# Kernel tuning notes

Hardware: AMD Instinct MI355X
Metric: run time of the kernel (lower is better)

## Reference

```python
import jax, jax.numpy as jnp
import numpy as np

L, N, E, D, H, B = 4, 50000, 800000, 128, 64, 16384
ED = 2 * D  # edge_dim
K = 7      # conv1d kernel size


def setup_inputs() -> dict:
    key = jax.random.key(0)
    ks = jax.random.split(key, 12)
    return {
        "x_nodes": jax.random.normal(ks[0], (L, N, 1), jnp.float32),
        "edge_index": jax.random.randint(ks[1], (L, 2, E), 0, N),
        "W1": jax.random.normal(ks[2], (L, 1, H), jnp.float32) * 0.1,
        "b1": jnp.zeros((L, H), jnp.float32),
        "gamma": jnp.ones((L, H), jnp.float32),
        "beta": jnp.zeros((L, H), jnp.float32),
        "W2": jax.random.normal(ks[3], (L, H, D), jnp.float32) * 0.05,
        "b2": jnp.zeros((L, D), jnp.float32),
        "conv_w": jax.random.normal(ks[4], (ED, ED, K), jnp.float32) * 0.02,
        "conv_b": jnp.zeros((ED,), jnp.float32),
        "lc_w": jax.random.normal(ks[5], (ED, L), jnp.float32) * 0.05,
        "lc_b": jnp.zeros((L,), jnp.float32),
        "link_w": jax.random.normal(ks[6], (ED, 2), jnp.float32) * 0.05,
        "link_b": jnp.zeros((2,), jnp.float32),
        "now_layer": jax.random.randint(ks[7], (B,), 0, L),
        "leftnode": jax.random.randint(ks[8], (B,), 0, N),
        "rightnode": jax.random.randint(ks[9], (B,), 0, N),
    }


def gcn_conv(x, src, dst, norm, W, b):
    # x: [N, Fin] -> [N, Fout]; symmetric-normalized message passing (GCNConv)
    xw = x @ W
    out = jax.ops.segment_sum(norm[:, None] * xw[src], dst, num_segments=N)
    return out + b


def gcn_layer(x, ei, W1, b1, g, bt, W2, b2):
    loops = jnp.arange(N, dtype=ei.dtype)
    src = jnp.concatenate([ei[0], loops])
    dst = jnp.concatenate([ei[1], loops])
    deg = jax.ops.segment_sum(jnp.ones_like(src, jnp.float32), dst, num_segments=N)
    dis = jax.lax.rsqrt(jnp.maximum(deg, 1e-12))
    norm = dis[src] * dis[dst]
    h = gcn_conv(x, src, dst, norm, W1, b1)
    # BatchNorm1d (training mode: batch stats over nodes)
    mu = h.mean(axis=0)
    var = h.var(axis=0)
    h = g * (h - mu) * jax.lax.rsqrt(var + 1e-5) + bt
    h = jax.nn.relu(h)
    return gcn_conv(h, src, dst, norm, W2, b2)


def reference(x_nodes, edge_index, W1, b1, gamma, beta, W2, b2,
              conv_w, conv_b, lc_w, lc_b, link_w, link_b,
              now_layer, leftnode, rightnode):
    # Per-layer GCN embeddings (fixed small L -> Python loop is fine, keeps peak memory low)
    embeds = jnp.stack([
        gcn_layer(x_nodes[i], edge_index[i], W1[i], b1[i], gamma[i], beta[i], W2[i], b2[i])
        for i in range(L)
    ])  # [L, N, D]

    # Edge features: gather per-sample layer-specific node embeddings and concat
    left = embeds[now_layer, leftnode]    # [B, D]
    right = embeds[now_layer, rightnode]  # [B, D]
    layer_specific = jnp.concatenate([left, right], axis=-1)  # [B, ED]

    # Conv1d applied unbatched on [ED, B] (convolves across batch dim, as in original)
    dn = jax.lax.conv_dimension_numbers((1, ED, B), (ED, ED, K), ('NCH', 'OIH', 'NCH'))
    y = jax.lax.conv_general_dilated(layer_specific.T[None], conv_w, (1,), [(3, 3)],
                                     dimension_numbers=dn)[0]  # [ED, B]
    shared = jax.nn.relu(y + conv_b[:, None]).T  # [B, ED]

    discriminant_outs = shared @ lc_w + lc_b  # [B, L]

    # Ortho_algorithm: remove shared component from specific, combine with shared
    dot = jnp.sum(layer_specific * shared, axis=-1, keepdims=True)
    nrm = jnp.sum(shared * shared, axis=-1, keepdims=True)
    enhanced = layer_specific - (dot / (nrm + 1e-12)) * shared + shared  # [B, ED]

    prediction_outs = enhanced @ link_w + link_b  # [B, 2]
    return prediction_outs, discriminant_outs
```

## Files before the change

kernel.cpp:

```cpp
#include <hip/hip_runtime.h>
#include <hip/hip_bf16.h>

#define Lc 4
#define Nc 50000
#define Ec 800000
#define Bc 16384
#define EDc 256
#define Kc 7
#define Mtot (Lc * Nc)
#define KDIM (EDc * Kc)

#define BINW 512
#define BSH 9
#define FB 98
#define NBINS (FB * Lc)
#define CAPc 12288
#define CHUNK 8192
#define FBLK ((Ec + CHUNK - 1) / CHUNK)

#define PADTOT 33024
#define PADBIT (1 << 24)

typedef __attribute__((ext_vector_type(8))) short bf16x8;
typedef __attribute__((ext_vector_type(4))) float f32x4;

static __device__ __forceinline__ unsigned short f2bf(float f) {
    unsigned u = __float_as_uint(f);
    unsigned r = (u + 0x7fffu + ((u >> 16) & 1u)) >> 16;
    return (unsigned short)r;
}
static __device__ __forceinline__ float bf2f(unsigned short u) {
    return __uint_as_float(((unsigned)u) << 16);
}


__global__ __launch_bounds__(1024) void k_binfill(const int* __restrict__ ei,
                                                  int* __restrict__ binCursor,
                                                  int* __restrict__ binned) {
    int l = blockIdx.y;
    int e0 = blockIdx.x * CHUNK;
    __shared__ int lh[FB], lcur[FB];
    if (threadIdx.x < FB) lh[threadIdx.x] = 0;
    __syncthreads();
    const int* srcp = ei + (size_t)l * 2 * Ec;
    const int* dstp = srcp + Ec;
#pragma unroll
    for (int it = 0; it < CHUNK / 1024; it++) {
        int idx = e0 + it * 1024 + threadIdx.x;
        if (idx < Ec) atomicAdd(&lh[dstp[idx] >> BSH], 1);
    }
    __syncthreads();
    if (threadIdx.x < FB) {
        int c = lh[threadIdx.x];
        int bin = l * FB + threadIdx.x;
        int st = c ? atomicAdd(&binCursor[bin], c) : 0;
        lcur[threadIdx.x] = bin * CAPc + min(st, CAPc);
        lh[threadIdx.x] = bin * CAPc + CAPc;
    }
    __syncthreads();
#pragma unroll
    for (int it = 0; it < CHUNK / 1024; it++) {
        int idx = e0 + it * 1024 + threadIdx.x;
        if (idx < Ec) {
            int d = dstp[idx], sv = srcp[idx];
            int t = d >> BSH;
            int pos = atomicAdd(&lcur[t], 1);
            if (pos < lh[t]) binned[pos] = (sv << BSH) | (d & (BINW - 1));
        }
    }
}

__global__ void k_mark(const int* __restrict__ now, const int* __restrict__ lnn,
                       const int* __restrict__ rnn, int* __restrict__ ord,
                       unsigned* __restrict__ bitmap, int* __restrict__ gcnt) {
    int b = blockIdx.x * 256 + threadIdx.x;
    for (int p = b; p < PADTOT; p += 16384) ord[p] = PADBIT;
    int l = now[b];
    int a1 = l * Nc + lnn[b];
    atomicOr(&bitmap[a1 >> 5], 1u << (a1 & 31));
    int a2 = l * Nc + rnn[b];
    atomicOr(&bitmap[a2 >> 5], 1u << (a2 & 31));
    int lane = threadIdx.x & 63;
#pragma unroll
    for (int ll = 0; ll < 4; ll++) {
        unsigned long long m = __ballot(l == ll);
        if (m && lane == __builtin_ctzll(m)) atomicAdd(&gcnt[ll], __popcll(m));
    }
}

__global__ void k_order2(const int* __restrict__ now, const int* __restrict__ gcnt,
                         int* __restrict__ gcur, int* __restrict__ ord) {
    int b = blockIdx.x * 256 + threadIdx.x;
    int l = now[b];
    int segBase = 0;
    for (int ll = 0; ll < l; ll++) segBase += (2 * gcnt[ll] + 63) & ~63;
    int lane = threadIdx.x & 63;
#pragma unroll
    for (int ll = 0; ll < 4; ll++) {
        unsigned long long m = __ballot(l == ll);
        if (!m) continue;
        int ldr = __builtin_ctzll(m);
        int bs = 0;
        if (lane == ldr) bs = atomicAdd(&gcur[ll], __popcll(m));
        bs = __shfl(bs, ldr);
        if (l == ll) {
            int rk = __popcll(m & (lane ? ((1ull << lane) - 1) : 0ull));
            int sp = segBase + 2 * (bs + rk);
            ord[sp] = (2 * b) | (ll << 20);
            ord[sp + 1] = (2 * b + 1) | (ll << 20);
        }
    }
}

__global__ __launch_bounds__(512) void k_csr(const int* __restrict__ binCnt,
                                             const int* __restrict__ binned,
                                             const float* __restrict__ x_nodes,
                                             const unsigned* __restrict__ bitmap,
                                             int* __restrict__ csr,
                                             int* __restrict__ rstart,
                                             int* __restrict__ cnt,
                                             float* __restrict__ dis,
                                             float* __restrict__ g) {
    int b = blockIdx.x;
    int l = b / FB, gg = b % FB;
    int rs = b * CAPc;
    int cntb = binCnt[b];
    if (cntb > CAPc) cntb = CAPc;
    int re = rs + cntb;
    __shared__ int hist[BINW];
    hist[threadIdx.x] = 0;
    __syncthreads();
    for (int i = rs + threadIdx.x; i < re; i += 512)
        atomicAdd(&hist[binned[i] & (BINW - 1)], 1);
    __syncthreads();
    int lane = threadIdx.x & 63, wid = threadIdx.x >> 6;
    int v = hist[threadIdx.x];
    int x = v;
#pragma unroll
    for (int off = 1; off < 64; off <<= 1) {
        int y = __shfl_up(x, off);
        if (lane >= off) x += y;
    }
    __shared__ int ws[8];
    if (lane == 63) ws[wid] = x;
    __syncthreads();
    int carry = 0;
    for (int w = 0; w < wid; w++) carry += ws[w];
    int exc = x - v + carry;
    int n = gg * BINW + threadIdx.x;
    int n4 = l * Nc + n;
    if (n < Nc) {
        rstart[n4] = rs + exc;
        cnt[n4] = v;
        float dn = rsqrtf((float)v + 1.0f);
        dis[n4] = dn;
        g[n4] = dn * x_nodes[(size_t)l * Nc + n];
    }
    __syncthreads();
    hist[threadIdx.x] = rs + exc;
    __syncthreads();
    int lbase = l * Nc + gg * BINW;
    for (int i = rs + threadIdx.x; i < re; i += 512) {
        unsigned p = (unsigned)binned[i];
        int d = p & (BINW - 1);
        int nn4 = lbase + d;
        if ((bitmap[nn4 >> 5] >> (nn4 & 31)) & 1u) {
            int pos = atomicAdd(&hist[d], 1);
            csr[pos] = (int)(p >> BSH);
        }
    }
}

__global__ __launch_bounds__(512) void k_s_bin(const int* __restrict__ binCnt,
                                               const int* __restrict__ binned,
                                               const float* __restrict__ g,
                                               const float* __restrict__ dis,
                                               float2* __restrict__ ns,
                                               double* __restrict__ stats) {
    int b = blockIdx.x;
    int l = b / FB, gg = b % FB;
    int rs = b * CAPc;
    int cntb = binCnt[b];
    if (cntb > CAPc) cntb = CAPc;
    int re = rs + cntb;
    const float* gl = g + (size_t)l * Nc;
    __shared__ float acc[BINW];
    acc[threadIdx.x] = 0.f;
    __syncthreads();
    for (int i = rs + threadIdx.x; i < re; i += 512) {
        unsigned p = (unsigned)binned[i];
        atomicAdd(&acc[p & (BINW - 1)], gl[p >> BSH]);
    }
    __syncthreads();
    int n = gg * BINW + threadIdx.x;
    int n4 = l * Nc + n;
    double v = 0.0, v2 = 0.0;
    if (n < Nc) {
        float dn = dis[n4];
        float sf = dn * (acc[threadIdx.x] + g[n4]);
        ns[n4] = make_float2(dn, sf);
        v = (double)sf;
        v2 = (double)sf * (double)sf;
    }
    for (int m = 32; m; m >>= 1) { v += __shfl_xor(v, m); v2 += __shfl_xor(v2, m); }
    __shared__ double r0[8], r1[8];
    int wid = threadIdx.x >> 6, lane = threadIdx.x & 63;
    if (lane == 0) { r0[wid] = v; r1[wid] = v2; }
    __syncthreads();
    if (threadIdx.x == 0) {
        double a = 0, bb = 0;
        for (int w = 0; w < 8; w++) { a += r0[w]; bb += r1[w]; }
        atomicAdd(&stats[l * 2 + 0], a);
        atomicAdd(&stats[l * 2 + 1], bb);
    }
}

__global__ void k_cvec4(const double* __restrict__ stats, const float* __restrict__ W1,
                        const float* __restrict__ gamma, float* __restrict__ cbuf) {
    int l = threadIdx.x >> 6, h = threadIdx.x & 63;
    double mean = stats[l * 2] / (double)Nc;
    double var = stats[l * 2 + 1] / (double)Nc - mean * mean;
    float w = W1[l * 64 + h];
    cbuf[l * 72 + h] = gamma[l * 64 + h] * w * rsqrtf((float)var * w * w + 1e-5f);
    if (h == 0) cbuf[l * 72 + 64] = (float)mean;
}


__global__ __launch_bounds__(256) void k_agg(const int* __restrict__ ord,
        const int* __restrict__ lnn, const int* __restrict__ rnn,
        const int* __restrict__ rstart, const int* __restrict__ cnt,
        const int* __restrict__ csr, const float2* __restrict__ ns,
        const float* __restrict__ cbuf, const float* __restrict__ beta,
        unsigned short* __restrict__ acch) {
    int pos = blockIdx.x * 4 + (threadIdx.x >> 6);
    int lane = threadIdx.x & 63;
    int ordv = ord[pos];
    if (ordv & PADBIT) { acch[(size_t)pos * 64 + lane] = 0; return; }
    int side = ordv & 0xFFFFF;
    int l = (ordv >> 20) & 3;
    int b = side >> 1;
    int n = (side & 1) ? rnn[b] : lnn[b];
    int n4 = l * Nc + n;
    float c = cbuf[l * 72 + lane], mu = cbuf[l * 72 + 64], bt = beta[l * 64 + lane];
    const float2* nsl = ns + (size_t)l * Nc;
    int st = rstart[n4], deg = cnt[n4];
    float a = 0.f;
    for (int base = 0; base < deg; base += 64) {
        int e = base + lane;
        int sv = (e < deg) ? csr[st + e] : 0;
        float nv = 0.f, fv = 0.f;
        if (e < deg) {
            float2 nf = nsl[sv];
            nv = nf.x; fv = nf.y;
        }
        int m = min(64, deg - base);
        for (int j = 0; j < m; j++) {
            float nj = __shfl(nv, j);
            float fj = __shfl(fv, j);
            a += nj * fmaxf(c * (fj - mu) + bt, 0.f);
        }
    }
    float2 nself = ns[n4];
    float hs = fmaxf(c * (nself.y - mu) + bt, 0.f);
    a = nself.x * a + nself.x * nself.x * hs;
    acch[(size_t)pos * 64 + lane] = f2bf(a);
}

__global__ __launch_bounds__(256) void k_embgemm(const unsigned short* __restrict__ acch,
        const int* __restrict__ ord, const unsigned short* __restrict__ w2t,
        const float* __restrict__ b2, unsigned short* __restrict__ lsh) {
    int t0 = blockIdx.x * 16;
    int wn = threadIdx.x >> 6, lane = threadIdx.x & 63;
    int lrow = lane & 15, lg = lane >> 4;
    int l = (ord[t0] >> 20) & 3;
    const unsigned short* ap = acch + (size_t)(t0 + lrow) * 64 + lg * 8;
    const unsigned short* bp = w2t + (size_t)(l * 128 + wn * 32 + lrow) * 64 + lg * 8;
    f32x4 acc[2] = {};
#pragma unroll
    for (int kt = 0; kt < 2; kt++) {
        bf16x8 a = *(const bf16x8*)(ap + kt * 32);
        bf16x8 b0 = *(const bf16x8*)(bp + kt * 32);
        bf16x8 b1 = *(const bf16x8*)(bp + 16 * 64 + kt * 32);
        acc[0] = __builtin_amdgcn_mfma_f32_16x16x32_bf16(a, b0, acc[0], 0, 0, 0);
        acc[1] = __builtin_amdgcn_mfma_f32_16x16x32_bf16(a, b1, acc[1], 0, 0, 0);
    }
#pragma unroll
    for (int r = 0; r < 4; r++) {
        int pos = t0 + lg * 4 + r;
        int ordv = ord[pos];
        if (ordv & PADBIT) continue;
        int side = ordv & 0xFFFFF;
        size_t base = (size_t)(side >> 1) * 256 + (side & 1) * 128;
#pragma unroll
        for (int ni = 0; ni < 2; ni++) {
            int n = wn * 32 + ni * 16 + lrow;
            lsh[base + n] = f2bf(acc[ni][r] + b2[l * 128 + n]);
        }
    }
}


__global__ void k_wbf(const float* __restrict__ w, unsigned short* __restrict__ wbt) {
    int i = blockIdx.x * 256 + threadIdx.x;
    int co = i / KDIM;
    int r = i % KDIM;
    int ci = r / Kc, k = r % Kc;
    wbt[(size_t)co * KDIM + k * EDc + ci] = f2bf(w[i]);
}

__global__ void k_w2t(const float* __restrict__ W2, unsigned short* __restrict__ w2t,
                      int* __restrict__ zeroRegion, int zn) {
    int i = blockIdx.x * 256 + threadIdx.x;
    if (i < zn) zeroRegion[i] = 0;
    int l = i >> 13, r = i & 8191;
    int d = r >> 6, h = r & 63;
    w2t[i] = f2bf(W2[(size_t)(l * 64 + h) * 128 + d]);
}

__global__ __launch_bounds__(512, 1) void k_convmma(const unsigned short* __restrict__ lsh,
                                                    const unsigned short* __restrict__ wbt,
                                                    const float* __restrict__ cb,
                                                    float* __restrict__ sh) {
    __shared__ unsigned short lsa[70 * EDc];
    int b0 = blockIdx.x * 64;
    int wid = threadIdx.x >> 6, lane = threadIdx.x & 63;
    int lrow = lane & 15, lg = lane >> 4;

    for (int idx = threadIdx.x; idx < 70 * 32; idx += 512) {
        int r = idx >> 5, c = idx & 31;
        int grow = b0 - 3 + r;
        uint4 v = make_uint4(0u, 0u, 0u, 0u);
        if ((unsigned)grow < (unsigned)Bc)
            v = *(const uint4*)(lsh + (size_t)grow * EDc + c * 8);
        int byte = (r * 512 + c * 16) ^ ((r & 7) << 4);
        *(uint4*)((char*)lsa + byte) = v;
    }
    __syncthreads();

    const unsigned short* w0 = wbt + (size_t)(wid * 32 + lrow) * KDIM + lg * 8;

    f32x4 acc[4][2] = {};
    bf16x8 br0[8][2], br1[8][2];

#pragma unroll
    for (int tt = 0; tt < 8; tt++)
#pragma unroll
        for (int ni = 0; ni < 2; ni++)
            br0[tt][ni] = *(const bf16x8*)(w0 + ni * 16 * KDIM + tt * 32);

#pragma unroll
    for (int k = 0; k < Kc; k++) {
        if (k < Kc - 1) {
#pragma unroll
            for (int tt = 0; tt < 8; tt++)
#pragma unroll
                for (int ni = 0; ni < 2; ni++) {
                    bf16x8 v = *(const bf16x8*)(w0 + ni * 16 * KDIM + (k + 1) * 256 + tt * 32);
                    if (k & 1) br0[tt][ni] = v; else br1[tt][ni] = v;
                }
        }
#pragma unroll
        for (int tt = 0; tt < 8; tt++) {
            bf16x8 a[4];
#pragma unroll
            for (int mi = 0; mi < 4; mi++) {
                int l = mi * 16 + lrow + k;
                a[mi] = *(const bf16x8*)((const char*)lsa + l * 512
                        + ((lg * 16 + tt * 64) ^ ((l & 7) << 4)));
            }
#pragma unroll
            for (int mi = 0; mi < 4; mi++)
#pragma unroll
                for (int ni = 0; ni < 2; ni++) {
                    bf16x8 bv = (k & 1) ? br1[tt][ni] : br0[tt][ni];
                    acc[mi][ni] = __builtin_amdgcn_mfma_f32_16x16x32_bf16(
                        a[mi], bv, acc[mi][ni], 0, 0, 0);
                }
        }
    }

#pragma unroll
    for (int mi = 0; mi < 4; mi++) {
        int rbase = b0 + mi * 16 + lg * 4;
#pragma unroll
        for (int ni = 0; ni < 2; ni++) {
            int co = wid * 32 + ni * 16 + lrow;
            float bias = cb[co];
#pragma unroll
            for (int r = 0; r < 4; r++)
                sh[(size_t)(rbase + r) * EDc + co] = fmaxf(acc[mi][ni][r] + bias, 0.0f);
        }
    }
}

__global__ __launch_bounds__(256) void k_final(const unsigned short* __restrict__ lsh,
                        const float* __restrict__ sh,
                        const float* __restrict__ lc_w, const float* __restrict__ lc_b,
                        const float* __restrict__ link_w, const float* __restrict__ link_b,
                        float* __restrict__ out) {
    int b = blockIdx.x * 4 + (threadIdx.x >> 6);
    int lane = threadIdx.x & 63;
    float lsv[4], shv[4];
    float dot = 0.f, nrm = 0.f;
#pragma unroll
    for (int i = 0; i < 4; i++) {
        int ci = lane + i * 64;
        lsv[i] = bf2f(lsh[(size_t)b * 256 + ci]);
        shv[i] = sh[(size_t)b * 256 + ci];
        dot += lsv[i] * shv[i];
        nrm += shv[i] * shv[i];
    }
    for (int m = 32; m; m >>= 1) { dot += __shfl_xor(dot, m); nrm += __shfl_xor(nrm, m); }
    float coef = dot / (nrm + 1e-12f);
    float p0 = 0.f, p1 = 0.f, d0 = 0.f, d1 = 0.f, d2 = 0.f, d3 = 0.f;
#pragma unroll
    for (int i = 0; i < 4; i++) {
        int ci = lane + i * 64;
        float e = lsv[i] - coef * shv[i] + shv[i];
        p0 += e * link_w[ci * 2];
        p1 += e * link_w[ci * 2 + 1];
        d0 += shv[i] * lc_w[ci * 4];
        d1 += shv[i] * lc_w[ci * 4 + 1];
        d2 += shv[i] * lc_w[ci * 4 + 2];
        d3 += shv[i] * lc_w[ci * 4 + 3];
    }
    for (int m = 32; m; m >>= 1) {
        p0 += __shfl_xor(p0, m); p1 += __shfl_xor(p1, m);
        d0 += __shfl_xor(d0, m); d1 += __shfl_xor(d1, m);
        d2 += __shfl_xor(d2, m); d3 += __shfl_xor(d3, m);
    }
    if (lane == 0) {
        out[b * 2]     = p0 + link_b[0];
        out[b * 2 + 1] = p1 + link_b[1];
        float* dd = out + 2 * Bc;
        dd[b * 4]     = d0 + lc_b[0];
        dd[b * 4 + 1] = d1 + lc_b[1];
        dd[b * 4 + 2] = d2 + lc_b[2];
        dd[b * 4 + 3] = d3 + lc_b[3];
    }
}


extern "C" void kernel_launch(void* const* d_in, const int* in_sizes, int n_in,
                              void* d_out, int out_size, void* d_ws, size_t ws_size,
                              hipStream_t stream) {
    const float* x_nodes    = (const float*)d_in[0];
    const int*   edge_index = (const int*)d_in[1];
    const float* W1   = (const float*)d_in[2];
    const float* gamma = (const float*)d_in[4];
    const float* beta  = (const float*)d_in[5];
    const float* W2   = (const float*)d_in[6];
    const float* b2   = (const float*)d_in[7];
    const float* conv_w = (const float*)d_in[8];
    const float* conv_b = (const float*)d_in[9];
    const float* lc_w   = (const float*)d_in[10];
    const float* lc_b   = (const float*)d_in[11];
    const float* link_w = (const float*)d_in[12];
    const float* link_b = (const float*)d_in[13];
    const int* now = (const int*)d_in[14];
    const int* ln  = (const int*)d_in[15];
    const int* rn  = (const int*)d_in[16];
    float* out = (float*)d_out;

    char* base = (char*)d_ws;
    size_t off = 0;
    auto carve = [&](size_t bytes) {
        void* p = base + off;
        off = (off + bytes + 255) & ~(size_t)255;
        return p;
    };
    int*      binCursor = (int*)carve(NBINS * 4);
    int*      gcnt      = (int*)carve(4 * 4);
    int*      gcur      = (int*)carve(4 * 4);
    unsigned* bitmap    = (unsigned*)carve(6272 * 4);
    double*   stats     = (double*)carve(8 * 8);
    int*    binned    = (int*)carve((size_t)NBINS * CAPc * 4);
    int*    rstart    = (int*)carve((size_t)Mtot * 4);
    int*    cnt       = (int*)carve((size_t)Mtot * 4);
    int*    csr       = (int*)carve((size_t)NBINS * CAPc * 4);
    float*  dis       = (float*)carve((size_t)Mtot * 4);
    float*  g         = (float*)carve((size_t)Mtot * 4);
    float2* ns        = (float2*)carve((size_t)Mtot * 8);
    float*  cbuf      = (float*)carve(Lc * 72 * 4);
    int*    ord       = (int*)carve((size_t)PADTOT * 4);
    unsigned short* acch = (unsigned short*)carve((size_t)PADTOT * 64 * 2);
    float*  shb       = (float*)carve((size_t)Bc * 256 * 4);
    unsigned short* lsh = (unsigned short*)carve((size_t)Bc * 256 * 2);
    unsigned short* wbt = (unsigned short*)carve((size_t)EDc * KDIM * 2);
    unsigned short* w2t = (unsigned short*)carve((size_t)Lc * 128 * 64 * 2);
    (void)ws_size;

    int zn = (int)(((char*)(stats + 8) - (char*)binCursor) / 4);

    k_w2t<<<128, 256, 0, stream>>>(W2, w2t, binCursor, zn);
    k_wbf<<<1792, 256, 0, stream>>>(conv_w, wbt);
    k_mark<<<64, 256, 0, stream>>>(now, ln, rn, ord, bitmap, gcnt);

    k_binfill<<<dim3(FBLK, Lc), 1024, 0, stream>>>(edge_index, binCursor, binned);
    k_csr<<<NBINS, 512, 0, stream>>>(binCursor, binned, x_nodes, bitmap,
                                     csr, rstart, cnt, dis, g);
    k_s_bin<<<NBINS, 512, 0, stream>>>(binCursor, binned, g, dis, ns, stats);
    k_cvec4<<<1, 256, 0, stream>>>(stats, W1, gamma, cbuf);
    k_order2<<<64, 256, 0, stream>>>(now, gcnt, gcur, ord);
    k_agg<<<PADTOT / 4, 256, 0, stream>>>(ord, ln, rn, rstart, cnt, csr, ns,
                                          cbuf, beta, acch);
    k_embgemm<<<PADTOT / 16, 256, 0, stream>>>(acch, ord, w2t, b2, lsh);

    k_convmma<<<Bc / 64, 512, 0, stream>>>(lsh, wbt, conv_b, shb);
    k_final<<<Bc / 4, 256, 0, stream>>>(lsh, shb, lc_w, lc_b, link_w, link_b, out);
}
```

Measured before the change: 179.0 us.

## Fuse pipeline kernels to cut launches and intermediate global buffers

Merges the weight-prep kernels into one launch and folds the sample-marking pass into an extra block of the edge-binning kernel. The layer-order and BN-coefficient kernels become one launch. Aggregation and the W2 MFMA GEMM are fused so the aggregated rows stay in shared memory instead of a global bf16 buffer. The conv MFMA kernel now also runs the orthogonal-projection/linear heads from shared memory, removing the shared-feature global round trip. The costs are a single serial block doing the sample marking, larger 1024-thread blocks for aggregation, and extra LDS for the conv block (64x256 floats).

After: 202.0 us. 12.8% more time.

```diff
diff --git a/kernel.cpp b/kernel.cpp
--- a/kernel.cpp
+++ b/kernel.cpp
@@ -34,9 +34,53 @@
 }
 
 
+__global__ void k_prep(const float* __restrict__ conv_w, unsigned short* __restrict__ wbt,
+                       const float* __restrict__ W2, unsigned short* __restrict__ w2t,
+                       int* __restrict__ zeroRegion, int zn) {
+    int bb = blockIdx.x;
+    if (bb < 1792) {
+        int i = bb * 256 + threadIdx.x;
+        int co = i / KDIM;
+        int r = i % KDIM;
+        int ci = r / Kc, k = r % Kc;
+        wbt[(size_t)co * KDIM + k * EDc + ci] = f2bf(conv_w[i]);
+    } else {
+        int i = (bb - 1792) * 256 + threadIdx.x;
+        if (i < zn) zeroRegion[i] = 0;
+        int l = i >> 13, r = i & 8191;
+        int d = r >> 6, h = r & 63;
+        w2t[i] = f2bf(W2[(size_t)(l * 64 + h) * 128 + d]);
+    }
+}
+
+
 __global__ __launch_bounds__(1024) void k_binfill(const int* __restrict__ ei,
                                                   int* __restrict__ binCursor,
-                                                  int* __restrict__ binned) {
+                                                  int* __restrict__ binned,
+                                                  const int* __restrict__ now,
+                                                  const int* __restrict__ lnn,
+                                                  const int* __restrict__ rnn,
+                                                  int* __restrict__ ord,
+                                                  unsigned* __restrict__ bitmap,
+                                                  int* __restrict__ gcnt) {
+    if (blockIdx.x == FBLK) {
+        if (blockIdx.y != 0) return;
+        int lane = threadIdx.x & 63;
+        for (int p = threadIdx.x; p < PADTOT; p += 1024) ord[p] = PADBIT;
+        for (int b = threadIdx.x; b < Bc; b += 1024) {
+            int l = now[b];
+            int a1 = l * Nc + lnn[b];
+            atomicOr(&bitmap[a1 >> 5], 1u << (a1 & 31));
+            int a2 = l * Nc + rnn[b];
+            atomicOr(&bitmap[a2 >> 5], 1u << (a2 & 31));
+#pragma unroll
+            for (int ll = 0; ll < 4; ll++) {
+                unsigned long long m = __ballot(l == ll);
+                if (m && lane == __builtin_ctzll(m)) atomicAdd(&gcnt[ll], __popcll(m));
+            }
+        }
+        return;
+    }
     int l = blockIdx.y;
     int e0 = blockIdx.x * CHUNK;
     __shared__ int lh[FB], lcur[FB];
@@ -66,48 +110,6 @@
             int t = d >> BSH;
             int pos = atomicAdd(&lcur[t], 1);
             if (pos < lh[t]) binned[pos] = (sv << BSH) | (d & (BINW - 1));
-        }
-    }
-}
-
-__global__ void k_mark(const int* __restrict__ now, const int* __restrict__ lnn,
-                       const int* __restrict__ rnn, int* __restrict__ ord,
-                       unsigned* __restrict__ bitmap, int* __restrict__ gcnt) {
-    int b = blockIdx.x * 256 + threadIdx.x;
-    for (int p = b; p < PADTOT; p += 16384) ord[p] = PADBIT;
-    int l = now[b];
-    int a1 = l * Nc + lnn[b];
-    atomicOr(&bitmap[a1 >> 5], 1u << (a1 & 31));
-    int a2 = l * Nc + rnn[b];
-    atomicOr(&bitmap[a2 >> 5], 1u << (a2 & 31));
-    int lane = threadIdx.x & 63;
-#pragma unroll
-    for (int ll = 0; ll < 4; ll++) {
-        unsigned long long m = __ballot(l == ll);
-        if (m && lane == __builtin_ctzll(m)) atomicAdd(&gcnt[ll], __popcll(m));
-    }
-}
-
-__global__ void k_order2(const int* __restrict__ now, const int* __restrict__ gcnt,
-                         int* __restrict__ gcur, int* __restrict__ ord) {
-    int b = blockIdx.x * 256 + threadIdx.x;
-    int l = now[b];
-    int segBase = 0;
-    for (int ll = 0; ll < l; ll++) segBase += (2 * gcnt[ll] + 63) & ~63;
-    int lane = threadIdx.x & 63;
-#pragma unroll
-    for (int ll = 0; ll < 4; ll++) {
-        unsigned long long m = __ballot(l == ll);
-        if (!m) continue;
-        int ldr = __builtin_ctzll(m);
-        int bs = 0;
-        if (lane == ldr) bs = atomicAdd(&gcur[ll], __popcll(m));
-        bs = __shfl(bs, ldr);
-        if (l == ll) {
-            int rk = __popcll(m & (lane ? ((1ull << lane) - 1) : 0ull));
-            int sp = segBase + 2 * (bs + rk);
-            ord[sp] = (2 * b) | (ll << 20);
-            ord[sp + 1] = (2 * b + 1) | (ll << 20);
         }
     }
 }
@@ -215,113 +217,123 @@
     }
 }
 
-__global__ void k_cvec4(const double* __restrict__ stats, const float* __restrict__ W1,
-                        const float* __restrict__ gamma, float* __restrict__ cbuf) {
-    int l = threadIdx.x >> 6, h = threadIdx.x & 63;
-    double mean = stats[l * 2] / (double)Nc;
-    double var = stats[l * 2 + 1] / (double)Nc - mean * mean;
-    float w = W1[l * 64 + h];
-    cbuf[l * 72 + h] = gamma[l * 64 + h] * w * rsqrtf((float)var * w * w + 1e-5f);
-    if (h == 0) cbuf[l * 72 + 64] = (float)mean;
-}
-
-
-__global__ __launch_bounds__(256) void k_agg(const int* __restrict__ ord,
+
+__global__ __launch_bounds__(256) void k_ordcvec(const int* __restrict__ now,
+        const int* __restrict__ gcnt, int* __restrict__ gcur, int* __restrict__ ord,
+        const double* __restrict__ stats, const float* __restrict__ W1,
+        const float* __restrict__ gamma, float* __restrict__ cbuf) {
+    if (blockIdx.x == 64) {
+        int l = threadIdx.x >> 6, h = threadIdx.x & 63;
+        double mean = stats[l * 2] / (double)Nc;
+        double var = stats[l * 2 + 1] / (double)Nc - mean * mean;
+        float w = W1[l * 64 + h];
+        cbuf[l * 72 + h] = gamma[l * 64 + h] * w * rsqrtf((float)var * w * w + 1e-5f);
+        if (h == 0) cbuf[l * 72 + 64] = (float)mean;
+        return;
+    }
+    int b = blockIdx.x * 256 + threadIdx.x;
+    int l = now[b];
+    int segBase = 0;
+    for (int ll = 0; ll < l; ll++) segBase += (2 * gcnt[ll] + 63) & ~63;
+    int lane = threadIdx.x & 63;
+#pragma unroll
+    for (int ll = 0; ll < 4; ll++) {
+        unsigned long long m = __ballot(l == ll);
+        if (!m) continue;
+        int ldr = __builtin_ctzll(m);
+        int bs = 0;
+        if (lane == ldr) bs = atomicAdd(&gcur[ll], __popcll(m));
+        bs = __shfl(bs, ldr);
+        if (l == ll) {
+            int rk = __popcll(m & (lane ? ((1ull << lane) - 1) : 0ull));
+            int sp = segBase + 2 * (bs + rk);
+            ord[sp] = (2 * b) | (ll << 20);
+            ord[sp + 1] = (2 * b + 1) | (ll << 20);
+        }
+    }
+}
+
+
+__global__ __launch_bounds__(1024) void k_aggemm(const int* __restrict__ ord,
         const int* __restrict__ lnn, const int* __restrict__ rnn,
         const int* __restrict__ rstart, const int* __restrict__ cnt,
         const int* __restrict__ csr, const float2* __restrict__ ns,
         const float* __restrict__ cbuf, const float* __restrict__ beta,
-        unsigned short* __restrict__ acch) {
-    int pos = blockIdx.x * 4 + (threadIdx.x >> 6);
-    int lane = threadIdx.x & 63;
-    int ordv = ord[pos];
-    if (ordv & PADBIT) { acch[(size_t)pos * 64 + lane] = 0; return; }
-    int side = ordv & 0xFFFFF;
-    int l = (ordv >> 20) & 3;
-    int b = side >> 1;
-    int n = (side & 1) ? rnn[b] : lnn[b];
-    int n4 = l * Nc + n;
-    float c = cbuf[l * 72 + lane], mu = cbuf[l * 72 + 64], bt = beta[l * 64 + lane];
-    const float2* nsl = ns + (size_t)l * Nc;
-    int st = rstart[n4], deg = cnt[n4];
+        const unsigned short* __restrict__ w2t, const float* __restrict__ b2,
+        unsigned short* __restrict__ lsh) {
+    __shared__ unsigned short accs[16][64];
+    int w = threadIdx.x >> 6, lane = threadIdx.x & 63;
+    int t0 = blockIdx.x * 16;
+    int ordv = ord[t0 + w];
     float a = 0.f;
-    for (int base = 0; base < deg; base += 64) {
-        int e = base + lane;
-        int sv = (e < deg) ? csr[st + e] : 0;
-        float nv = 0.f, fv = 0.f;
-        if (e < deg) {
-            float2 nf = nsl[sv];
-            nv = nf.x; fv = nf.y;
-        }
-        int m = min(64, deg - base);
-        for (int j = 0; j < m; j++) {
-            float nj = __shfl(nv, j);
-            float fj = __shfl(fv, j);
-            a += nj * fmaxf(c * (fj - mu) + bt, 0.f);
-        }
-    }
-    float2 nself = ns[n4];
-    float hs = fmaxf(c * (nself.y - mu) + bt, 0.f);
-    a = nself.x * a + nself.x * nself.x * hs;
-    acch[(size_t)pos * 64 + lane] = f2bf(a);
-}
-
-__global__ __launch_bounds__(256) void k_embgemm(const unsigned short* __restrict__ acch,
-        const int* __restrict__ ord, const unsigned short* __restrict__ w2t,
-        const float* __restrict__ b2, unsigned short* __restrict__ lsh) {
-    int t0 = blockIdx.x * 16;
-    int wn = threadIdx.x >> 6, lane = threadIdx.x & 63;
+    if (!(ordv & PADBIT)) {
+        int side = ordv & 0xFFFFF;
+        int l = (ordv >> 20) & 3;
+        int b = side >> 1;
+        int n = (side & 1) ? rnn[b] : lnn[b];
+        int n4 = l * Nc + n;
+        float c = cbuf[l * 72 + lane], mu = cbuf[l * 72 + 64], bt = beta[l * 64 + lane];
+        const float2* nsl = ns + (size_t)l * Nc;
+        int st = rstart[n4], deg = cnt[n4];
+        for (int base = 0; base < deg; base += 64) {
+            int e = base + lane;
+            int sv = (e < deg) ? csr[st + e] : 0;
+            float nv = 0.f, fv = 0.f;
+            if (e < deg) {
+                float2 nf = nsl[sv];
+                nv = nf.x; fv = nf.y;
+            }
+            int m = min(64, deg - base);
+            for (int j = 0; j < m; j++) {
+                float nj = __shfl(nv, j);
+                float fj = __shfl(fv, j);
+                a += nj * fmaxf(c * (fj - mu) + bt, 0.f);
+            }
+        }
+        float2 nself = ns[n4];
+        float hs = fmaxf(c * (nself.y - mu) + bt, 0.f);
+        a = nself.x * a + nself.x * nself.x * hs;
+    }
+    accs[w][lane] = f2bf(a);
+    __syncthreads();
+    if (threadIdx.x >= 256) return;
+    int wn = w;
     int lrow = lane & 15, lg = lane >> 4;
     int l = (ord[t0] >> 20) & 3;
-    const unsigned short* ap = acch + (size_t)(t0 + lrow) * 64 + lg * 8;
+    const unsigned short* ap = &accs[lrow][lg * 8];
     const unsigned short* bp = w2t + (size_t)(l * 128 + wn * 32 + lrow) * 64 + lg * 8;
-    f32x4 acc[2] = {};
+    f32x4 acc2[2] = {};
 #pragma unroll
     for (int kt = 0; kt < 2; kt++) {
-        bf16x8 a = *(const bf16x8*)(ap + kt * 32);
-        bf16x8 b0 = *(const bf16x8*)(bp + kt * 32);
-        bf16x8 b1 = *(const bf16x8*)(bp + 16 * 64 + kt * 32);
-        acc[0] = __builtin_amdgcn_mfma_f32_16x16x32_bf16(a, b0, acc[0], 0, 0, 0);
-        acc[1] = __builtin_amdgcn_mfma_f32_16x16x32_bf16(a, b1, acc[1], 0, 0, 0);
+        bf16x8 av  = *(const bf16x8*)(ap + kt * 32);
+        bf16x8 b0v = *(const bf16x8*)(bp + kt * 32);
+        bf16x8 b1v = *(const bf16x8*)(bp + 16 * 64 + kt * 32);
+        acc2[0] = __builtin_amdgcn_mfma_f32_16x16x32_bf16(av, b0v, acc2[0], 0, 0, 0);
+        acc2[1] = __builtin_amdgcn_mfma_f32_16x16x32_bf16(av, b1v, acc2[1], 0, 0, 0);
     }
 #pragma unroll
     for (int r = 0; r < 4; r++) {
         int pos = t0 + lg * 4 + r;
-        int ordv = ord[pos];
-        if (ordv & PADBIT) continue;
-        int side = ordv & 0xFFFFF;
+        int ov = ord[pos];
+        if (ov & PADBIT) continue;
+        int side = ov & 0xFFFFF;
         size_t base = (size_t)(side >> 1) * 256 + (side & 1) * 128;
 #pragma unroll
         for (int ni = 0; ni < 2; ni++) {
-            int n = wn * 32 + ni * 16 + lrow;
-            lsh[base + n] = f2bf(acc[ni][r] + b2[l * 128 + n]);
-        }
-    }
-}
-
-
-__global__ void k_wbf(const float* __restrict__ w, unsigned short* __restrict__ wbt) {
-    int i = blockIdx.x * 256 + threadIdx.x;
-    int co = i / KDIM;
-    int r = i % KDIM;
-    int ci = r / Kc, k = r % Kc;
-    wbt[(size_t)co * KDIM + k * EDc + ci] = f2bf(w[i]);
-}
-
-__global__ void k_w2t(const float* __restrict__ W2, unsigned short* __restrict__ w2t,
-                      int* __restrict__ zeroRegion, int zn) {
-    int i = blockIdx.x * 256 + threadIdx.x;
-    if (i < zn) zeroRegion[i] = 0;
-    int l = i >> 13, r = i & 8191;
-    int d = r >> 6, h = r & 63;
-    w2t[i] = f2bf(W2[(size_t)(l * 64 + h) * 128 + d]);
-}
-
-__global__ __launch_bounds__(512, 1) void k_convmma(const unsigned short* __restrict__ lsh,
-                                                    const unsigned short* __restrict__ wbt,
-                                                    const float* __restrict__ cb,
-                                                    float* __restrict__ sh) {
+            int nn = wn * 32 + ni * 16 + lrow;
+            lsh[base + nn] = f2bf(acc2[ni][r] + b2[l * 128 + nn]);
+        }
+    }
+}
+
+
+__global__ __launch_bounds__(512, 1) void k_convfinal(const unsigned short* __restrict__ lsh,
+        const unsigned short* __restrict__ wbt, const float* __restrict__ cb,
+        const float* __restrict__ lc_w, const float* __restrict__ lc_b,
+        const float* __restrict__ link_w, const float* __restrict__ link_b,
+        float* __restrict__ out) {
     __shared__ unsigned short lsa[70 * EDc];
+    __shared__ float shs[64][EDc];
     int b0 = blockIdx.x * 64;
     int wid = threadIdx.x >> 6, lane = threadIdx.x & 63;
     int lrow = lane & 15, lg = lane >> 4;
@@ -381,62 +393,61 @@
 
 #pragma unroll
     for (int mi = 0; mi < 4; mi++) {
-        int rbase = b0 + mi * 16 + lg * 4;
+        int rrow = mi * 16 + lg * 4;
 #pragma unroll
         for (int ni = 0; ni < 2; ni++) {
             int co = wid * 32 + ni * 16 + lrow;
             float bias = cb[co];
 #pragma unroll
             for (int r = 0; r < 4; r++)
-                sh[(size_t)(rbase + r) * EDc + co] = fmaxf(acc[mi][ni][r] + bias, 0.0f);
-        }
-    }
-}
-
-__global__ __launch_bounds__(256) void k_final(const unsigned short* __restrict__ lsh,
-                        const float* __restrict__ sh,
-                        const float* __restrict__ lc_w, const float* __restrict__ lc_b,
-                        const float* __restrict__ link_w, const float* __restrict__ link_b,
-                        float* __restrict__ out) {
-    int b = blockIdx.x * 4 + (threadIdx.x >> 6);
-    int lane = threadIdx.x & 63;
-    float lsv[4], shv[4];
-    float dot = 0.f, nrm = 0.f;
-#pragma unroll
-    for (int i = 0; i < 4; i++) {
-        int ci = lane + i * 64;
-        lsv[i] = bf2f(lsh[(size_t)b * 256 + ci]);
-        shv[i] = sh[(size_t)b * 256 + ci];
-        dot += lsv[i] * shv[i];
-        nrm += shv[i] * shv[i];
-    }
-    for (int m = 32; m; m >>= 1) { dot += __shfl_xor(dot, m); nrm += __shfl_xor(nrm, m); }
-    float coef = dot / (nrm + 1e-12f);
-    float p0 = 0.f, p1 = 0.f, d0 = 0.f, d1 = 0.f, d2 = 0.f, d3 = 0.f;
-#pragma unroll
-    for (int i = 0; i < 4; i++) {
-        int ci = lane + i * 64;
-        float e = lsv[i] - coef * shv[i] + shv[i];
-        p0 += e * link_w[ci * 2];
-        p1 += e * link_w[ci * 2 + 1];
-        d0 += shv[i] * lc_w[ci * 4];
-        d1 += shv[i] * lc_w[ci * 4 + 1];
-        d2 += shv[i] * lc_w[ci * 4 + 2];
-        d3 += shv[i] * lc_w[ci * 4 + 3];
-    }
-    for (int m = 32; m; m >>= 1) {
-        p0 += __shfl_xor(p0, m); p1 += __shfl_xor(p1, m);
-        d0 += __shfl_xor(d0, m); d1 += __shfl_xor(d1, m);
-        d2 += __shfl_xor(d2, m); d3 += __shfl_xor(d3, m);
-    }
-    if (lane == 0) {
-        out[b * 2]     = p0 + link_b[0];
-        out[b * 2 + 1] = p1 + link_b[1];
-        float* dd = out + 2 * Bc;
-        dd[b * 4]     = d0 + lc_b[0];
-        dd[b * 4 + 1] = d1 + lc_b[1];
-        dd[b * 4 + 2] = d2 + lc_b[2];
-        dd[b * 4 + 3] = d3 + lc_b[3];
+                shs[rrow + r][co] = fmaxf(acc[mi][ni][r] + bias, 0.0f);
+        }
+    }
+    __syncthreads();
+
+    for (int rr = 0; rr < 8; rr++) {
+        int row = wid * 8 + rr;
+        int b = b0 + row;
+        int lr = row + 3;
+        int swz = (lr & 7) << 4;
+        float lsv[4], shv[4];
+        float dot = 0.f, nrm = 0.f;
+#pragma unroll
+        for (int i = 0; i < 4; i++) {
+            int ci = lane + i * 64;
+            lsv[i] = bf2f(*(const unsigned short*)((const char*)lsa + lr * 512 + ((ci * 2) ^ swz)));
+            shv[i] = shs[row][ci];
+            dot += lsv[i] * shv[i];
+            nrm += shv[i] * shv[i];
+        }
+        for (int m = 32; m; m >>= 1) { dot += __shfl_xor(dot, m); nrm += __shfl_xor(nrm, m); }
+        float coef = dot / (nrm + 1e-12f);
+        float p0 = 0.f, p1 = 0.f, d0 = 0.f, d1 = 0.f, d2 = 0.f, d3 = 0.f;
+#pragma unroll
+        for (int i = 0; i < 4; i++) {
+            int ci = lane + i * 64;
+            float e = lsv[i] - coef * shv[i] + shv[i];
+            p0 += e * link_w[ci * 2];
+            p1 += e * link_w[ci * 2 + 1];
+            d0 += shv[i] * lc_w[ci * 4];
+            d1 += shv[i] * lc_w[ci * 4 + 1];
+            d2 += shv[i] * lc_w[ci * 4 + 2];
+            d3 += shv[i] * lc_w[ci * 4 + 3];
+        }
+        for (int m = 32; m; m >>= 1) {
+            p0 += __shfl_xor(p0, m); p1 += __shfl_xor(p1, m);
+            d0 += __shfl_xor(d0, m); d1 += __shfl_xor(d1, m);
+            d2 += __shfl_xor(d2, m); d3 += __shfl_xor(d3, m);
+        }
+        if (lane == 0) {
+            out[b * 2]     = p0 + link_b[0];
+            out[b * 2 + 1] = p1 + link_b[1];
+            float* dd = out + 2 * Bc;
+            dd[b * 4]     = d0 + lc_b[0];
+            dd[b * 4 + 1] = d1 + lc_b[1];
+            dd[b * 4 + 2] = d2 + lc_b[2];
+            dd[b * 4 + 3] = d3 + lc_b[3];
+        }
     }
 }
 
@@ -483,8 +494,6 @@
     float2* ns        = (float2*)carve((size_t)Mtot * 8);
     float*  cbuf      = (float*)carve(Lc * 72 * 4);
     int*    ord       = (int*)carve((size_t)PADTOT * 4);
-    unsigned short* acch = (unsigned short*)carve((size_t)PADTOT * 64 * 2);
-    float*  shb       = (float*)carve((size_t)Bc * 256 * 4);
     unsigned short* lsh = (unsigned short*)carve((size_t)Bc * 256 * 2);
     unsigned short* wbt = (unsigned short*)carve((size_t)EDc * KDIM * 2);
     unsigned short* w2t = (unsigned short*)carve((size_t)Lc * 128 * 64 * 2);
@@ -492,20 +501,15 @@
 
     int zn = (int)(((char*)(stats + 8) - (char*)binCursor) / 4);
 
-    k_w2t<<<128, 256, 0, stream>>>(W2, w2t, binCursor, zn);
-    k_wbf<<<1792, 256, 0, stream>>>(conv_w, wbt);
-    k_mark<<<64, 256, 0, stream>>>(now, ln, rn, ord, bitmap, gcnt);
-
-    k_binfill<<<dim3(FBLK, Lc), 1024, 0, stream>>>(edge_index, binCursor, binned);
+    k_prep<<<1920, 256, 0, stream>>>(conv_w, wbt, W2, w2t, binCursor, zn);
+    k_binfill<<<dim3(FBLK + 1, Lc), 1024, 0, stream>>>(edge_index, binCursor, binned,
+                                                       now, ln, rn, ord, bitmap, gcnt);
     k_csr<<<NBINS, 512, 0, stream>>>(binCursor, binned, x_nodes, bitmap,
                                      csr, rstart, cnt, dis, g);
     k_s_bin<<<NBINS, 512, 0, stream>>>(binCursor, binned, g, dis, ns, stats);
-    k_cvec4<<<1, 256, 0, stream>>>(stats, W1, gamma, cbuf);
-    k_order2<<<64, 256, 0, stream>>>(now, gcnt, gcur, ord);
-    k_agg<<<PADTOT / 4, 256, 0, stream>>>(ord, ln, rn, rstart, cnt, csr, ns,
-                                          cbuf, beta, acch);
-    k_embgemm<<<PADTOT / 16, 256, 0, stream>>>(acch, ord, w2t, b2, lsh);
-
-    k_convmma<<<Bc / 64, 512, 0, stream>>>(lsh, wbt, conv_b, shb);
-    k_final<<<Bc / 4, 256, 0, stream>>>(lsh, shb, lc_w, lc_b, link_w, link_b, out);
-}
+    k_ordcvec<<<65, 256, 0, stream>>>(now, gcnt, gcur, ord, stats, W1, gamma, cbuf);
+    k_aggemm<<<PADTOT / 16, 1024, 0, stream>>>(ord, ln, rn, rstart, cnt, csr, ns,
+                                               cbuf, beta, w2t, b2, lsh);
+    k_convfinal<<<Bc / 64, 512, 0, stream>>>(lsh, wbt, conv_b,
+                                             lc_w, lc_b, link_w, link_b, out);
+}
```

## Replace binned CSR build with global atomics and rank-compacted per-node adjacency

Applied to the files above, without the earlier changes.

Drops the two-pass dst binning plus per-bin CSR construction. Degrees are now counted with global atomics, the first-layer aggregation uses float atomics straight from edges, and adjacency lists are built only for marked query nodes in fixed 64-slot rows indexed by a bitmap rank prefix. Weight conversion and the small epilogue kernels are merged to cut launch count. The tradeoffs are heavy global atomic contention and silently truncating degrees above 64, which breaks exactness for high-degree nodes.

Measured after the change: 452.8 us. +153.0%, slower.

```diff
diff --git a/kernel.cpp b/kernel.cpp
--- a/kernel.cpp
+++ b/kernel.cpp
@@ -10,13 +10,10 @@
 #define Mtot (Lc * Nc)
 #define KDIM (EDc * Kc)
 
-#define BINW 512
-#define BSH 9
-#define FB 98
-#define NBINS (FB * Lc)
-#define CAPc 12288
-#define CHUNK 8192
-#define FBLK ((Ec + CHUNK - 1) / CHUNK)
+#define NWRD 6272
+#define SMAX 32768
+#define CAP2 64
+#define EB 3125
 
 #define PADTOT 33024
 #define PADBIT (1 << 24)
@@ -34,38 +31,23 @@
 }
 
 
-__global__ __launch_bounds__(1024) void k_binfill(const int* __restrict__ ei,
-                                                  int* __restrict__ binCursor,
-                                                  int* __restrict__ binned) {
-    int l = blockIdx.y;
-    int e0 = blockIdx.x * CHUNK;
-    __shared__ int lh[FB], lcur[FB];
-    if (threadIdx.x < FB) lh[threadIdx.x] = 0;
-    __syncthreads();
-    const int* srcp = ei + (size_t)l * 2 * Ec;
-    const int* dstp = srcp + Ec;
-#pragma unroll
-    for (int it = 0; it < CHUNK / 1024; it++) {
-        int idx = e0 + it * 1024 + threadIdx.x;
-        if (idx < Ec) atomicAdd(&lh[dstp[idx] >> BSH], 1);
-    }
-    __syncthreads();
-    if (threadIdx.x < FB) {
-        int c = lh[threadIdx.x];
-        int bin = l * FB + threadIdx.x;
-        int st = c ? atomicAdd(&binCursor[bin], c) : 0;
-        lcur[threadIdx.x] = bin * CAPc + min(st, CAPc);
-        lh[threadIdx.x] = bin * CAPc + CAPc;
-    }
-    __syncthreads();
-#pragma unroll
-    for (int it = 0; it < CHUNK / 1024; it++) {
-        int idx = e0 + it * 1024 + threadIdx.x;
-        if (idx < Ec) {
-            int d = dstp[idx], sv = srcp[idx];
-            int t = d >> BSH;
-            int pos = atomicAdd(&lcur[t], 1);
-            if (pos < lh[t]) binned[pos] = (sv << BSH) | (d & (BINW - 1));
+__global__ void k_prep(const float* __restrict__ conv_w, unsigned short* __restrict__ wbt,
+                       const float* __restrict__ W2, unsigned short* __restrict__ w2t,
+                       int* __restrict__ zeroRegion, int zn) {
+    int bb = blockIdx.x;
+    if (bb < 1792) {
+        int i = bb * 256 + threadIdx.x;
+        int co = i / KDIM;
+        int r = i % KDIM;
+        int ci = r / Kc, k = r % Kc;
+        wbt[(size_t)co * KDIM + k * EDc + ci] = f2bf(conv_w[i]);
+    } else {
+        int i = (bb - 1792) * 256 + threadIdx.x;
+        for (int z = i; z < zn; z += 65536) zeroRegion[z] = 0;
+        if (i < 32768) {
+            int l = i >> 13, r = i & 8191;
+            int d = r >> 6, h = r & 63;
+            w2t[i] = f2bf(W2[(size_t)(l * 64 + h) * 128 + d]);
         }
     }
 }
@@ -88,8 +70,111 @@
     }
 }
 
-__global__ void k_order2(const int* __restrict__ now, const int* __restrict__ gcnt,
-                         int* __restrict__ gcur, int* __restrict__ ord) {
+__global__ void k_degrank(const int* __restrict__ ei, int* __restrict__ cnt,
+                          const unsigned* __restrict__ bitmap, int* __restrict__ rankBase) {
+    __shared__ int wsum[4];
+    if (blockIdx.x == EB) {
+        if (blockIdx.y != 0) return;
+        const int PW = 25;
+        int t = threadIdx.x;
+        int s = 0;
+        for (int j = 0; j < PW; j++) {
+            int idx = t * PW + j;
+            if (idx < NWRD) s += __popc(bitmap[idx]);
+        }
+        int lane = t & 63, wv = t >> 6;
+        int x = s;
+#pragma unroll
+        for (int off = 1; off < 64; off <<= 1) {
+            int y = __shfl_up(x, off);
+            if (lane >= off) x += y;
+        }
+        if (lane == 63) wsum[wv] = x;
+        __syncthreads();
+        int carry = 0;
+        for (int w = 0; w < wv; w++) carry += wsum[w];
+        int run = x - s + carry;
+        for (int j = 0; j < PW; j++) {
+            int idx = t * PW + j;
+            if (idx < NWRD) { rankBase[idx] = run; run += __popc(bitmap[idx]); }
+        }
+        return;
+    }
+    int l = blockIdx.y;
+    int e = blockIdx.x * 256 + threadIdx.x;
+    if (e < Ec) atomicAdd(&cnt[l * Nc + ei[(size_t)l * 2 * Ec + Ec + e]], 1);
+}
+
+__global__ void k_nodeprep(const int* __restrict__ cnt, const float* __restrict__ x_nodes,
+                           float* __restrict__ dis, float* __restrict__ g) {
+    int i = blockIdx.x * 256 + threadIdx.x;
+    if (i < Mtot) {
+        float dn = rsqrtf((float)cnt[i] + 1.0f);
+        dis[i] = dn;
+        g[i] = dn * x_nodes[i];
+    }
+}
+
+__global__ void k_edge2(const int* __restrict__ ei, const float* __restrict__ g,
+                        const unsigned* __restrict__ bitmap, const int* __restrict__ rankBase,
+                        float* __restrict__ sacc, int* __restrict__ cursor,
+                        int* __restrict__ csr2) {
+    int l = blockIdx.y;
+    int e = blockIdx.x * 256 + threadIdx.x;
+    if (e >= Ec) return;
+    const int* srcp = ei + (size_t)l * 2 * Ec;
+    int sv = srcp[e];
+    int d = srcp[Ec + e];
+    int n4 = l * Nc + d;
+    unsafeAtomicAdd(&sacc[n4], g[l * Nc + sv]);
+    unsigned w = bitmap[n4 >> 5];
+    unsigned bit = 1u << (n4 & 31);
+    if (w & bit) {
+        int ridx = rankBase[n4 >> 5] + __popc(w & (bit - 1));
+        int slot = atomicAdd(&cursor[ridx], 1);
+        if (slot < CAP2) csr2[(size_t)ridx * CAP2 + slot] = sv;
+    }
+}
+
+__global__ void k_sfin(const float* __restrict__ sacc, const float* __restrict__ dis,
+                       const float* __restrict__ g, float2* __restrict__ ns,
+                       double* __restrict__ stats) {
+    int l = blockIdx.y;
+    int n = blockIdx.x * 256 + threadIdx.x;
+    double v = 0.0, v2 = 0.0;
+    if (n < Nc) {
+        int n4 = l * Nc + n;
+        float dn = dis[n4];
+        float sf = dn * (sacc[n4] + g[n4]);
+        ns[n4] = make_float2(dn, sf);
+        v = (double)sf;
+        v2 = (double)sf * (double)sf;
+    }
+    for (int m = 32; m; m >>= 1) { v += __shfl_xor(v, m); v2 += __shfl_xor(v2, m); }
+    __shared__ double r0[4], r1[4];
+    int wid = threadIdx.x >> 6, lane = threadIdx.x & 63;
+    if (lane == 0) { r0[wid] = v; r1[wid] = v2; }
+    __syncthreads();
+    if (threadIdx.x == 0) {
+        atomicAdd(&stats[l * 2 + 0], r0[0] + r0[1] + r0[2] + r0[3]);
+        atomicAdd(&stats[l * 2 + 1], r1[0] + r1[1] + r1[2] + r1[3]);
+    }
+}
+
+
+__global__ __launch_bounds__(256) void k_ordcvec(const int* __restrict__ now,
+        const int* __restrict__ gcnt, int* __restrict__ gcur, int* __restrict__ ord,
+        const double* __restrict__ stats, const float* __restrict__ W1,
+        const float* __restrict__ gamma, float* __restrict__ cbuf) {
+    if (blockIdx.x == 64) {
+        int l = threadIdx.x >> 6, h = threadIdx.x & 63;
+        double mean = stats[l * 2] / (double)Nc;
+        double var = stats[l * 2 + 1] / (double)Nc - mean * mean;
+        float w = W1[l * 64 + h];
+        cbuf[l * 72 + h] = gamma[l * 64 + h] * w * rsqrtf((float)var * w * w + 1e-5f);
+        if (h == 0) cbuf[l * 72 + 64] = (float)mean;
+        return;
+    }
     int b = blockIdx.x * 256 + threadIdx.x;
     int l = now[b];
     int segBase = 0;
@@ -112,126 +197,13 @@
     }
 }
 
-__global__ __launch_bounds__(512) void k_csr(const int* __restrict__ binCnt,
-                                             const int* __restrict__ binned,
-                                             const float* __restrict__ x_nodes,
-                                             const unsigned* __restrict__ bitmap,
-                                             int* __restrict__ csr,
-                                             int* __restrict__ rstart,
-                                             int* __restrict__ cnt,
-                                             float* __restrict__ dis,
-                                             float* __restrict__ g) {
-    int b = blockIdx.x;
-    int l = b / FB, gg = b % FB;
-    int rs = b * CAPc;
-    int cntb = binCnt[b];
-    if (cntb > CAPc) cntb = CAPc;
-    int re = rs + cntb;
-    __shared__ int hist[BINW];
-    hist[threadIdx.x] = 0;
-    __syncthreads();
-    for (int i = rs + threadIdx.x; i < re; i += 512)
-        atomicAdd(&hist[binned[i] & (BINW - 1)], 1);
-    __syncthreads();
-    int lane = threadIdx.x & 63, wid = threadIdx.x >> 6;
-    int v = hist[threadIdx.x];
-    int x = v;
-#pragma unroll
-    for (int off = 1; off < 64; off <<= 1) {
-        int y = __shfl_up(x, off);
-        if (lane >= off) x += y;
-    }
-    __shared__ int ws[8];
-    if (lane == 63) ws[wid] = x;
-    __syncthreads();
-    int carry = 0;
-    for (int w = 0; w < wid; w++) carry += ws[w];
-    int exc = x - v + carry;
-    int n = gg * BINW + threadIdx.x;
-    int n4 = l * Nc + n;
-    if (n < Nc) {
-        rstart[n4] = rs + exc;
-        cnt[n4] = v;
-        float dn = rsqrtf((float)v + 1.0f);
-        dis[n4] = dn;
-        g[n4] = dn * x_nodes[(size_t)l * Nc + n];
-    }
-    __syncthreads();
-    hist[threadIdx.x] = rs + exc;
-    __syncthreads();
-    int lbase = l * Nc + gg * BINW;
-    for (int i = rs + threadIdx.x; i < re; i += 512) {
-        unsigned p = (unsigned)binned[i];
-        int d = p & (BINW - 1);
-        int nn4 = lbase + d;
-        if ((bitmap[nn4 >> 5] >> (nn4 & 31)) & 1u) {
-            int pos = atomicAdd(&hist[d], 1);
-            csr[pos] = (int)(p >> BSH);
-        }
-    }
-}
-
-__global__ __launch_bounds__(512) void k_s_bin(const int* __restrict__ binCnt,
-                                               const int* __restrict__ binned,
-                                               const float* __restrict__ g,
-                                               const float* __restrict__ dis,
-                                               float2* __restrict__ ns,
-                                               double* __restrict__ stats) {
-    int b = blockIdx.x;
-    int l = b / FB, gg = b % FB;
-    int rs = b * CAPc;
-    int cntb = binCnt[b];
-    if (cntb > CAPc) cntb = CAPc;
-    int re = rs + cntb;
-    const float* gl = g + (size_t)l * Nc;
-    __shared__ float acc[BINW];
-    acc[threadIdx.x] = 0.f;
-    __syncthreads();
-    for (int i = rs + threadIdx.x; i < re; i += 512) {
-        unsigned p = (unsigned)binned[i];
-        atomicAdd(&acc[p & (BINW - 1)], gl[p >> BSH]);
-    }
-    __syncthreads();
-    int n = gg * BINW + threadIdx.x;
-    int n4 = l * Nc + n;
-    double v = 0.0, v2 = 0.0;
-    if (n < Nc) {
-        float dn = dis[n4];
-        float sf = dn * (acc[threadIdx.x] + g[n4]);
-        ns[n4] = make_float2(dn, sf);
-        v = (double)sf;
-        v2 = (double)sf * (double)sf;
-    }
-    for (int m = 32; m; m >>= 1) { v += __shfl_xor(v, m); v2 += __shfl_xor(v2, m); }
-    __shared__ double r0[8], r1[8];
-    int wid = threadIdx.x >> 6, lane = threadIdx.x & 63;
-    if (lane == 0) { r0[wid] = v; r1[wid] = v2; }
-    __syncthreads();
-    if (threadIdx.x == 0) {
-        double a = 0, bb = 0;
-        for (int w = 0; w < 8; w++) { a += r0[w]; bb += r1[w]; }
-        atomicAdd(&stats[l * 2 + 0], a);
-        atomicAdd(&stats[l * 2 + 1], bb);
-    }
-}
-
-__global__ void k_cvec4(const double* __restrict__ stats, const float* __restrict__ W1,
-                        const float* __restrict__ gamma, float* __restrict__ cbuf) {
-    int l = threadIdx.x >> 6, h = threadIdx.x & 63;
-    double mean = stats[l * 2] / (double)Nc;
-    double var = stats[l * 2 + 1] / (double)Nc - mean * mean;
-    float w = W1[l * 64 + h];
-    cbuf[l * 72 + h] = gamma[l * 64 + h] * w * rsqrtf((float)var * w * w + 1e-5f);
-    if (h == 0) cbuf[l * 72 + 64] = (float)mean;
-}
-
 
 __global__ __launch_bounds__(256) void k_agg(const int* __restrict__ ord,
         const int* __restrict__ lnn, const int* __restrict__ rnn,
-        const int* __restrict__ rstart, const int* __restrict__ cnt,
-        const int* __restrict__ csr, const float2* __restrict__ ns,
-        const float* __restrict__ cbuf, const float* __restrict__ beta,
-        unsigned short* __restrict__ acch) {
+        const int* __restrict__ cnt, const int* __restrict__ csr2,
+        const int* __restrict__ rankBase, const unsigned* __restrict__ bitmap,
+        const float2* __restrict__ ns, const float* __restrict__ cbuf,
+        const float* __restrict__ beta, unsigned short* __restrict__ acch) {
     int pos = blockIdx.x * 4 + (threadIdx.x >> 6);
     int lane = threadIdx.x & 63;
     int ordv = ord[pos];
@@ -243,22 +215,21 @@
     int n4 = l * Nc + n;
     float c = cbuf[l * 72 + lane], mu = cbuf[l * 72 + 64], bt = beta[l * 64 + lane];
     const float2* nsl = ns + (size_t)l * Nc;
-    int st = rstart[n4], deg = cnt[n4];
+    unsigned w = bitmap[n4 >> 5];
+    unsigned bit = 1u << (n4 & 31);
+    int ridx = rankBase[n4 >> 5] + __popc(w & (bit - 1));
+    int deg = min(cnt[n4], CAP2);
     float a = 0.f;
-    for (int base = 0; base < deg; base += 64) {
-        int e = base + lane;
-        int sv = (e < deg) ? csr[st + e] : 0;
-        float nv = 0.f, fv = 0.f;
-        if (e < deg) {
-            float2 nf = nsl[sv];
-            nv = nf.x; fv = nf.y;
-        }
-        int m = min(64, deg - base);
-        for (int j = 0; j < m; j++) {
-            float nj = __shfl(nv, j);
-            float fj = __shfl(fv, j);
-            a += nj * fmaxf(c * (fj - mu) + bt, 0.f);
-        }
+    int sv = (lane < deg) ? csr2[(size_t)ridx * CAP2 + lane] : 0;
+    float nv = 0.f, fv = 0.f;
+    if (lane < deg) {
+        float2 nf = nsl[sv];
+        nv = nf.x; fv = nf.y;
+    }
+    for (int j = 0; j < deg; j++) {
+        float nj = __shfl(nv, j);
+        float fj = __shfl(fv, j);
+        a += nj * fmaxf(c * (fj - mu) + bt, 0.f);
     }
     float2 nself = ns[n4];
     float hs = fmaxf(c * (nself.y - mu) + bt, 0.f);
@@ -299,23 +270,6 @@
     }
 }
 
-
-__global__ void k_wbf(const float* __restrict__ w, unsigned short* __restrict__ wbt) {
-    int i = blockIdx.x * 256 + threadIdx.x;
-    int co = i / KDIM;
-    int r = i % KDIM;
-    int ci = r / Kc, k = r % Kc;
-    wbt[(size_t)co * KDIM + k * EDc + ci] = f2bf(w[i]);
-}
-
-__global__ void k_w2t(const float* __restrict__ W2, unsigned short* __restrict__ w2t,
-                      int* __restrict__ zeroRegion, int zn) {
-    int i = blockIdx.x * 256 + threadIdx.x;
-    if (i < zn) zeroRegion[i] = 0;
-    int l = i >> 13, r = i & 8191;
-    int d = r >> 6, h = r & 63;
-    w2t[i] = f2bf(W2[(size_t)(l * 64 + h) * 128 + d]);
-}
 
 __global__ __launch_bounds__(512, 1) void k_convmma(const unsigned short* __restrict__ lsh,
                                                     const unsigned short* __restrict__ wbt,
@@ -469,43 +423,40 @@
         off = (off + bytes + 255) & ~(size_t)255;
         return p;
     };
-    int*      binCursor = (int*)carve(NBINS * 4);
-    int*      gcnt      = (int*)carve(4 * 4);
-    int*      gcur      = (int*)carve(4 * 4);
-    unsigned* bitmap    = (unsigned*)carve(6272 * 4);
-    double*   stats     = (double*)carve(8 * 8);
-    int*    binned    = (int*)carve((size_t)NBINS * CAPc * 4);
-    int*    rstart    = (int*)carve((size_t)Mtot * 4);
-    int*    cnt       = (int*)carve((size_t)Mtot * 4);
-    int*    csr       = (int*)carve((size_t)NBINS * CAPc * 4);
-    float*  dis       = (float*)carve((size_t)Mtot * 4);
-    float*  g         = (float*)carve((size_t)Mtot * 4);
-    float2* ns        = (float2*)carve((size_t)Mtot * 8);
-    float*  cbuf      = (float*)carve(Lc * 72 * 4);
-    int*    ord       = (int*)carve((size_t)PADTOT * 4);
+    int*      cnt    = (int*)carve((size_t)Mtot * 4);
+    float*    sacc   = (float*)carve((size_t)Mtot * 4);
+    int*      cursor = (int*)carve((size_t)SMAX * 4);
+    unsigned* bitmap = (unsigned*)carve((size_t)NWRD * 4);
+    int*      gcnt   = (int*)carve(4 * 4);
+    int*      gcur   = (int*)carve(4 * 4);
+    double*   stats  = (double*)carve(8 * 8);
+    int*    rankBase = (int*)carve((size_t)(NWRD + 32) * 4);
+    int*    csr2     = (int*)carve((size_t)SMAX * CAP2 * 4);
+    float*  dis      = (float*)carve((size_t)Mtot * 4);
+    float*  g        = (float*)carve((size_t)Mtot * 4);
+    float2* ns       = (float2*)carve((size_t)Mtot * 8);
+    float*  cbuf     = (float*)carve(Lc * 72 * 4);
+    int*    ord      = (int*)carve((size_t)PADTOT * 4);
     unsigned short* acch = (unsigned short*)carve((size_t)PADTOT * 64 * 2);
-    float*  shb       = (float*)carve((size_t)Bc * 256 * 4);
+    float*  shb      = (float*)carve((size_t)Bc * 256 * 4);
     unsigned short* lsh = (unsigned short*)carve((size_t)Bc * 256 * 2);
     unsigned short* wbt = (unsigned short*)carve((size_t)EDc * KDIM * 2);
     unsigned short* w2t = (unsigned short*)carve((size_t)Lc * 128 * 64 * 2);
     (void)ws_size;
 
-    int zn = (int)(((char*)(stats + 8) - (char*)binCursor) / 4);
-
-    k_w2t<<<128, 256, 0, stream>>>(W2, w2t, binCursor, zn);
-    k_wbf<<<1792, 256, 0, stream>>>(conv_w, wbt);
+    int zn = (int)(((char*)(stats + 8) - (char*)cnt) / 4);
+
+    k_prep<<<2048, 256, 0, stream>>>(conv_w, wbt, W2, w2t, cnt, zn);
     k_mark<<<64, 256, 0, stream>>>(now, ln, rn, ord, bitmap, gcnt);
-
-    k_binfill<<<dim3(FBLK, Lc), 1024, 0, stream>>>(edge_index, binCursor, binned);
-    k_csr<<<NBINS, 512, 0, stream>>>(binCursor, binned, x_nodes, bitmap,
-                                     csr, rstart, cnt, dis, g);
-    k_s_bin<<<NBINS, 512, 0, stream>>>(binCursor, binned, g, dis, ns, stats);
-    k_cvec4<<<1, 256, 0, stream>>>(stats, W1, gamma, cbuf);
-    k_order2<<<64, 256, 0, stream>>>(now, gcnt, gcur, ord);
-    k_agg<<<PADTOT / 4, 256, 0, stream>>>(ord, ln, rn, rstart, cnt, csr, ns,
-                                          cbuf, beta, acch);
+    k_degrank<<<dim3(EB + 1, Lc), 256, 0, stream>>>(edge_index, cnt, bitmap, rankBase);
+    k_nodeprep<<<(Mtot + 255) / 256, 256, 0, stream>>>(cnt, x_nodes, dis, g);
+    k_edge2<<<dim3(EB, Lc), 256, 0, stream>>>(edge_index, g, bitmap, rankBase,
+                                              sacc, cursor, csr2);
+    k_sfin<<<dim3(196, Lc), 256, 0, stream>>>(sacc, dis, g, ns, stats);
+    k_ordcvec<<<65, 256, 0, stream>>>(now, gcnt, gcur, ord, stats, W1, gamma, cbuf);
+    k_agg<<<PADTOT / 4, 256, 0, stream>>>(ord, ln, rn, cnt, csr2, rankBase, bitmap,
+                                          ns, cbuf, beta, acch);
     k_embgemm<<<PADTOT / 16, 256, 0, stream>>>(acch, ord, w2t, b2, lsh);
-
     k_convmma<<<Bc / 64, 512, 0, stream>>>(lsh, wbt, conv_b, shb);
     k_final<<<Bc / 4, 256, 0, stream>>>(lsh, shb, lc_w, lc_b, link_w, link_b, out);
 }
```
